# Kernel optimization log

Hardware: AMD Instinct MI355X
Metric: run time of the kernel (lower is better)

## Reference

```python
import jax, jax.numpy as jnp
import numpy as np
import math

WINDOW_SIZE = 11
SIGMA = 1.5
K1 = 0.01
K2 = 0.03
MAX_VAL = 1.0


def _make_window(window_size=WINDOW_SIZE, sigma=SIGMA):
    # Faithful to torch: 1D gaussian -> [1,1,window_size] -> repeat((3,1,1,1)) -> [3,1,1,ws]
    xs = np.arange(window_size)
    w = np.exp(-((xs - window_size // 2) ** 2) / float(2 * sigma ** 2)).astype(np.float32)
    w = w / w.sum()
    w = w[None, None, :]                      # [1,1,ws]
    w = np.tile(w[None], (3, 1, 1, 1))        # [3,1,1,ws]  (OIHW, 1x11 kernel, 3 out channels)
    return jnp.asarray(w)


def _conv(x, w, pad):
    # x: [B,1,H,W], w: [3,1,1,ws], padding=pad on both spatial dims (matches torch conv2d)
    return jax.lax.conv_general_dilated(
        x, w, window_strides=(1, 1), padding=((pad, pad), (pad, pad)),
        dimension_numbers=("NCHW", "OIHW", "NCHW"))


def setup_inputs() -> dict:
    key = jax.random.key(0)
    k1, k2 = jax.random.split(key)
    B, H, W = 16, 512, 512
    img1 = jax.random.uniform(k1, (B, H, W), dtype=jnp.float32)
    img2 = jax.random.uniform(k2, (B, H, W), dtype=jnp.float32)
    return {"img1": img1, "img2": img2}


def reference(img1, img2):
    pad = WINDOW_SIZE // 2
    window = _make_window()
    x1 = img1[:, None, :, :]  # [B,1,H,W]
    x2 = img2[:, None, :, :]

    mu1 = _conv(x1, window, pad)              # [B,3,H+2p,W]
    mu2 = _conv(x2, window, pad)
    mu1_mu2 = mu1 * mu2
    mu1_sq = mu1 * mu1
    mu2_sq = mu2 * mu2
    sigma1_sq = _conv(x1 * x1, window, pad) - mu1_sq
    sigma2_sq = _conv(x2 * x2, window, pad) - mu2_sq
    sigma12 = _conv(x1 * x2, window, pad) - mu1_mu2

    C1 = (K1 * MAX_VAL) ** 2
    C2 = (K2 * MAX_VAL) ** 2
    ssim = (2 * mu1_mu2 + C1) * (2 * sigma12 + C2) / (
        (mu1_sq + mu2_sq + C1) * (sigma1_sq + sigma2_sq + C2))
    return 1.0 - jnp.mean(ssim)
```

## Files before the change

### kernel.cpp

```cpp
#include <hip/hip_runtime.h>
#include <cmath>

typedef float f32x4 __attribute__((ext_vector_type(4)));

#define IMG_W 512
#define NROWS 8192
#define WPB 4
#define TPB (WPB * 64)
#define NBLOCKS (NROWS / WPB)

struct WinW { float w[11]; };

__global__ __launch_bounds__(TPB) void ssim_rows(
    const float* __restrict__ img1, const float* __restrict__ img2,
    float* __restrict__ partial, WinW ww)
{
    const int tid  = threadIdx.x;
    const int lane = tid & 63;
    const int wv   = tid >> 6;
    const int row  = blockIdx.x * WPB + wv;
    const long long base = (long long)row * IMG_W + lane * 8;

    const float C1 = 1e-4f;
    const float C2 = 9e-4f;

    const f32x4 a0 = *(const f32x4*)&img1[base];
    const f32x4 a1 = *(const f32x4*)&img1[base + 4];
    const f32x4 b0 = *(const f32x4*)&img2[base];
    const f32x4 b1 = *(const f32x4*)&img2[base + 4];

    float W1[18], W2[18];
    #pragma unroll
    for (int j = 0; j < 4; ++j) {
        W1[5 + j] = a0[j];  W1[9 + j] = a1[j];
        W2[5 + j] = b0[j];  W2[9 + j] = b1[j];
    }
    #pragma unroll
    for (int j = 0; j < 5; ++j) {
        const float u1 = __shfl_up(W1[8 + j], 1, 64);
        const float u2 = __shfl_up(W2[8 + j], 1, 64);
        W1[j] = (lane == 0) ? 0.f : u1;
        W2[j] = (lane == 0) ? 0.f : u2;
        const float d1 = __shfl_down(W1[5 + j], 1, 64);
        const float d2 = __shfl_down(W2[5 + j], 1, 64);
        W1[13 + j] = (lane == 63) ? 0.f : d1;
        W2[13 + j] = (lane == 63) ? 0.f : d2;
    }

    float AA[18], BB[18], AB[18];
    #pragma unroll
    for (int j = 0; j < 18; ++j) {
        AA[j] = W1[j] * W1[j];
        BB[j] = W2[j] * W2[j];
        AB[j] = W1[j] * W2[j];
    }

    float acc = 0.f;
    #pragma unroll
    for (int p = 0; p < 8; ++p) {
        float mu1 = 0.f, mu2 = 0.f, s11 = 0.f, s22 = 0.f, s12 = 0.f;
        #pragma unroll
        for (int k = 0; k < 11; ++k) {
            const float wk = ww.w[k];
            mu1 = fmaf(wk, W1[p + k], mu1);
            mu2 = fmaf(wk, W2[p + k], mu2);
            s11 = fmaf(wk, AA[p + k], s11);
            s22 = fmaf(wk, BB[p + k], s22);
            s12 = fmaf(wk, AB[p + k], s12);
        }
        const float m12 = mu1 * mu2;
        const float m1s = mu1 * mu1;
        const float m2s = mu2 * mu2;
        const float num = (2.f * m12 + C1) * (2.f * (s12 - m12) + C2);
        const float den = (m1s + m2s + C1) * ((s11 - m1s) + (s22 - m2s) + C2);
        acc += num * __builtin_amdgcn_rcpf(den);
    }

    #pragma unroll
    for (int off = 32; off > 0; off >>= 1)
        acc += __shfl_down(acc, off, 64);
    __shared__ float wsum[WPB];
    if (lane == 0) wsum[wv] = acc;
    __syncthreads();
    if (tid == 0) partial[blockIdx.x] = wsum[0] + wsum[1] + wsum[2] + wsum[3];
}

__global__ __launch_bounds__(256) void ssim_final(
    const float* __restrict__ partial, float* __restrict__ out)
{
    const int tid = threadIdx.x;
    float s = 0.f;
    for (int i = tid; i < NBLOCKS; i += 256) s += partial[i];
    #pragma unroll
    for (int off = 32; off > 0; off >>= 1)
        s += __shfl_down(s, off, 64);
    __shared__ float ws[4];
    if ((tid & 63) == 0) ws[tid >> 6] = s;
    __syncthreads();
    if (tid == 0) {
        const float total = ws[0] + ws[1] + ws[2] + ws[3];
        out[0] = 1.0f - (total + 81920.0f) / 4276224.0f;
    }
}

extern "C" void kernel_launch(void* const* d_in, const int* in_sizes, int n_in,
                              void* d_out, int out_size, void* d_ws, size_t ws_size,
                              hipStream_t stream) {
    const float* img1 = (const float*)d_in[0];
    const float* img2 = (const float*)d_in[1];
    float* out = (float*)d_out;
    float* partial = (float*)d_ws;

    WinW ww;
    for (int i = 0; i < 11; ++i) {
        const double d = (double)(i - 5);
        ww.w[i] = (float)std::exp(-(d * d) / 4.5);
    }
    float s = 0.f;
    for (int i = 0; i < 11; ++i) s += ww.w[i];
    for (int i = 0; i < 11; ++i) ww.w[i] /= s;

    ssim_rows<<<NBLOCKS, TPB, 0, stream>>>(img1, img2, partial, ww);
    ssim_final<<<1, 256, 0, stream>>>(partial, out);
}
```

Before: 17.86 us.

## Fuse final reduction into main kernel via fixed-point atomic last-block tree

Removes the second reduction kernel launch. Each block quantizes its partial sum to fixed point and atomically adds it, together with a packed arrival counter, into one of 8 cells. The last block into each cell forwards the cell total to a root counter, and the last arrival at the root writes the final SSIM value. This adds a memset launch, atomic contention on a few cache lines, and some quantization error from the fixed-point sums.

```diff
diff --git a/kernel.cpp b/kernel.cpp
--- a/kernel.cpp
+++ b/kernel.cpp
@@ -8,12 +8,15 @@
 #define WPB 4
 #define TPB (WPB * 64)
 #define NBLOCKS (NROWS / WPB)
+#define NCELLS 8
+#define CELL_QUOTA (NBLOCKS / NCELLS)
 
 struct WinW { float w[11]; };
 
-__global__ __launch_bounds__(TPB) void ssim_rows(
+
+__global__ __launch_bounds__(TPB) void ssim_fused(
     const float* __restrict__ img1, const float* __restrict__ img2,
-    float* __restrict__ partial, WinW ww)
+    unsigned long long* __restrict__ ws64, float* __restrict__ out, WinW ww)
 {
     const int tid  = threadIdx.x;
     const int lane = tid & 63;
@@ -82,24 +85,32 @@
     __shared__ float wsum[WPB];
     if (lane == 0) wsum[wv] = acc;
     __syncthreads();
-    if (tid == 0) partial[blockIdx.x] = wsum[0] + wsum[1] + wsum[2] + wsum[3];
-}
 
-__global__ __launch_bounds__(256) void ssim_final(
-    const float* __restrict__ partial, float* __restrict__ out)
-{
-    const int tid = threadIdx.x;
-    float s = 0.f;
-    for (int i = tid; i < NBLOCKS; i += 256) s += partial[i];
-    #pragma unroll
-    for (int off = 32; off > 0; off >>= 1)
-        s += __shfl_down(s, off, 64);
-    __shared__ float ws[4];
-    if ((tid & 63) == 0) ws[tid >> 6] = s;
-    __syncthreads();
     if (tid == 0) {
-        const float total = ws[0] + ws[1] + ws[2] + ws[3];
-        out[0] = 1.0f - (total + 81920.0f) / 4276224.0f;
+        const float sb = wsum[0] + wsum[1] + wsum[2] + wsum[3];
+        const double v = (double)sb * 16777216.0 + 68719476736.0 ;
+        const unsigned long long qp = (unsigned long long)(v + 0.5);
+
+        unsigned long long* cell = ws64 + (blockIdx.x & (NCELLS - 1)) * 8;
+        const unsigned long long cadd = qp + (1ULL << 55);
+        const unsigned long long cprev =
+            __hip_atomic_fetch_add(cell, cadd, __ATOMIC_RELAXED,
+                                   __HIP_MEMORY_SCOPE_AGENT);
+        if ((cprev >> 55) == CELL_QUOTA - 1) {
+            const unsigned long long csum =
+                (cprev + cadd) & ((1ULL << 55) - 1);
+            const unsigned long long radd = csum + (1ULL << 60);
+            const unsigned long long rprev =
+                __hip_atomic_fetch_add(ws64 + 64, radd, __ATOMIC_RELAXED,
+                                       __HIP_MEMORY_SCOPE_AGENT);
+            if ((rprev >> 60) == NCELLS - 1) {
+                const unsigned long long rsum =
+                    (rprev + radd) & ((1ULL << 60) - 1);
+                const long long q = (long long)rsum - (2048LL << 36);
+                const double total = (double)q / 16777216.0;
+                out[0] = (float)(1.0 - (total + 81920.0) / 4276224.0);
+            }
+        }
     }
 }
 
@@ -109,7 +120,9 @@
     const float* img1 = (const float*)d_in[0];
     const float* img2 = (const float*)d_in[1];
     float* out = (float*)d_out;
-    float* partial = (float*)d_ws;
+    unsigned long long* ws64 = (unsigned long long*)d_ws;
+
+    hipMemsetAsync(d_ws, 0, 576, stream);
 
     WinW ww;
     for (int i = 0; i < 11; ++i) {
@@ -120,6 +133,5 @@
     for (int i = 0; i < 11; ++i) s += ww.w[i];
     for (int i = 0; i < 11; ++i) ww.w[i] /= s;
 
-    ssim_rows<<<NBLOCKS, TPB, 0, stream>>>(img1, img2, partial, ww);
-    ssim_final<<<1, 256, 0, stream>>>(partial, out);
+    ssim_fused<<<NBLOCKS, TPB, 0, stream>>>(img1, img2, ws64, out, ww);
 }
```

New measurement: 20.41 us. 1.14x slower.
